# Kernel tuning notes

Measured on AMD Instinct MI355X. Metric: run time of the kernel, lower is better.

The kernel has to match this reference:

```python
import jax, jax.numpy as jnp
import numpy as np

N, IN_DIM, OUT_DIM, NUM_HOPS, SD = 8192, 256, 256, 4, 64
ETA, LAM_LAP, LAM_SP, EPS = 0.5, 0.3, 0.05, 0.5
LN_EPS = 1e-5


def setup_inputs() -> dict:
    key = jax.random.key(0)
    ks = jax.random.split(key, 6)
    K = NUM_HOPS + 1
    return {
        "H": jax.random.normal(ks[0], (N, IN_DIM), jnp.float32),
        "hops": jax.random.normal(ks[1], (K, N, IN_DIM), jnp.float32),
        "L": jax.random.normal(ks[2], (N, N), jnp.float32),
        "U": jax.random.normal(ks[3], (K, IN_DIM, SD), jnp.float32) * 0.1,
        "W_in": jax.random.normal(ks[4], (OUT_DIM, IN_DIM), jnp.float32) * 0.05,
        "ln_gamma": jnp.ones((OUT_DIM,), jnp.float32),
        "ln_beta": jnp.zeros((OUT_DIM,), jnp.float32),
        "log_tau": jnp.zeros((), jnp.float32),
    }


def _per_hop(U_k, H_k):
    n = H_k.shape[0]
    Q, _ = jnp.linalg.qr(U_k)                 # [in_dim, sd]
    Z = Q.T @ H_k.T                           # [sd, n]
    G = Z @ Z.T                               # [sd, sd] Gram, reused
    Sigma = G / (n + 1e-8)
    tr_S = jnp.trace(Sigma)
    tr_S2 = jnp.sum(Sigma * Sigma)            # trace(Sigma @ Sigma), Sigma symmetric
    rank_eff = tr_S ** 2 / (tr_S2 + 1e-8)
    coeff = SD / (n * EPS ** 2 + 1e-8)
    M = jnp.eye(SD, dtype=Z.dtype) + coeff * G
    Lc = jnp.linalg.cholesky(M)
    MiZ = jax.scipy.linalg.cho_solve((Lc, True), Z)  # [sd, n]
    grad_R = (Q @ MiZ).T                      # [n, in_dim]
    return rank_eff, grad_R


def reference(H, hops, L, U, W_in, ln_gamma, ln_beta, log_tau):
    tau = jnp.clip(jnp.exp(log_tau), 0.1, 10.0)
    rank_effs, grads_R = jax.vmap(_per_hop)(U, hops)      # [K], [K,n,in_dim]
    lap_terms = jnp.einsum('nm,kmd->knd', L, hops)        # [K,n,in_dim]
    w = jax.nn.softmax(rank_effs / tau)                   # [K]
    grad_sum = jnp.einsum('k,knd->nd', w, grads_R)
    lap_sum = jnp.einsum('k,knd->nd', w, lap_terms)
    H_half = H + ETA * grad_sum - ETA * LAM_LAP * lap_sum
    H_prox = jnp.sign(H_half) * jax.nn.relu(jnp.abs(H_half) - LAM_SP * ETA)
    H_out = H_prox @ W_in.T
    mu = jnp.mean(H_out, axis=-1, keepdims=True)
    var = jnp.var(H_out, axis=-1, keepdims=True)
    H_out = (H_out - mu) * jax.lax.rsqrt(var + LN_EPS) * ln_gamma + ln_beta
    return H_out, rank_effs, w
```

## Files before the change

### kernel.cpp

```cpp
#include <hip/hip_runtime.h>
#include <stdint.h>


typedef __attribute__((ext_vector_type(8))) short  s16x8;
typedef __attribute__((ext_vector_type(4))) float  f32x4;

#define NNODE 8192
#define DIN   256
#define KHOP  5
#define SDM   64

static const size_t OFF_Q    = 0;
static const size_t OFF_QT   = OFF_Q   + (size_t)5*256*64*4;
static const size_t OFF_ZT   = OFF_QT  + (size_t)5*64*256*2;
static const size_t OFF_GP   = OFF_ZT  + (size_t)5*8192*64*2;
static const size_t OFF_LM   = OFF_GP  + (size_t)5*16*4096*4;
static const size_t OFF_RD   = OFF_LM  + (size_t)5*4096*4;
static const size_t OFF_LU   = OFF_RD  + (size_t)5*64*4;
static const size_t OFF_RDU  = OFF_LU  + (size_t)5*4096*4;
static const size_t OFF_RE   = OFF_RDU + (size_t)5*64*4;
static const size_t OFF_W    = OFF_RE  + 64;
static const size_t OFF_T2   = OFF_W   + 64;
static const size_t OFF_HWT  = OFF_T2  + (size_t)5*256*64*2;
static const size_t OFF_WBF  = OFF_HWT + (size_t)256*8192*2;
static const size_t OFF_HP   = OFF_WBF + (size_t)256*256*2;
static const size_t OFF_PART = OFF_HP  + (size_t)8192*256*2;

__device__ __forceinline__ unsigned short f2bf(float f){
  unsigned u = __builtin_bit_cast(unsigned, f);
  u += 0x7FFFu + ((u >> 16) & 1u);
  return (unsigned short)(u >> 16);
}
__device__ __forceinline__ float bf2f(unsigned h){
  return __builtin_bit_cast(float, h << 16);
}
__device__ __forceinline__ void gl_lds16(const void* g, void* l){
  __builtin_amdgcn_global_load_lds(
      (const __attribute__((address_space(1))) void*)g,
      (__attribute__((address_space(3))) void*)l, 16, 0, 0);
}
__device__ __forceinline__ f32x4 mfma16(s16x8 a, s16x8 b, f32x4 c){
  return __builtin_amdgcn_mfma_f32_16x16x32_bf16(a, b, c, 0, 0, 0);
}

__device__ __forceinline__ void wave_chol64(float* a, float& rdk, int lane){
  rdk = 0.0f;
  #pragma unroll
  for (int j = 0; j < 64; ++j){
    float dj  = __shfl(a[j], j);
    float d   = sqrtf(fmaxf(dj, 1e-20f));
    float rdj = 1.0f / d;
    float cj  = a[j] * rdj;
    a[j] = cj;
    if (lane == j) rdk = rdj;
    #pragma unroll
    for (int l = j+1; l < 64; ++l)
      a[l] -= cj * __shfl(cj, l);
  }
}

__global__ __launch_bounds__(256) void k_pre(const float* __restrict__ U,
                                             float* __restrict__ Lu,
                                             float* __restrict__ rdu){
  __shared__ float A[64*65];
  int tid = threadIdx.x;
  int k = blockIdx.x;
  const float* Uk = U + (size_t)k*16384;
  int ti = tid >> 4, tj = tid & 15;
  float s[16];
  #pragma unroll
  for (int i = 0; i < 16; ++i) s[i] = 0.0f;
  for (int n = 0; n < 256; ++n){
    f32x4 xa = *(const f32x4*)(Uk + n*64 + ti*4);
    f32x4 xb = *(const f32x4*)(Uk + n*64 + tj*4);
    #pragma unroll
    for (int p = 0; p < 4; ++p)
      #pragma unroll
      for (int q = 0; q < 4; ++q) s[p*4+q] += xa[p]*xb[q];
  }
  #pragma unroll
  for (int p = 0; p < 4; ++p)
    #pragma unroll
    for (int q = 0; q < 4; ++q) A[(ti*4+p)*65 + tj*4+q] = s[p*4+q];
  __syncthreads();
  if (tid < 64){
    int lane = tid;
    float a[64];
    #pragma unroll
    for (int l = 0; l < 64; ++l) a[l] = A[lane*65 + l];
    float rdk;
    wave_chol64(a, rdk, lane);
    #pragma unroll
    for (int l = 0; l < 64; ++l) Lu[(size_t)k*4096 + lane*64 + l] = a[l];
    rdu[k*64 + lane] = rdk;
  }
}

__global__ __launch_bounds__(256) void k_qsolve(const float* __restrict__ U,
                                                const float* __restrict__ Lu,
                                                const float* __restrict__ rdu,
                                                float* __restrict__ Qf,
                                                unsigned short* __restrict__ Qt){
  int k = blockIdx.y, tid = threadIdx.x, wave = tid >> 6, lane = tid & 63;
  __shared__ float Al[64*65];
  __shared__ float rds[64];
  for (int e = tid; e < 4096; e += 256) Al[(e>>6)*65 + (e&63)] = Lu[(size_t)k*4096 + e];
  if (tid < 64) rds[tid] = rdu[k*64 + tid];
  __syncthreads();
  int n = blockIdx.x*4 + wave;
  float x = U[((size_t)k*256 + n)*64 + lane];
  #pragma unroll
  for (int j = 0; j < 64; ++j){
    float zj = __shfl(x, j) * rds[j];
    x = (lane == j) ? zj : (lane > j ? x - Al[lane*65+j]*zj : x);
  }
  Qf[((size_t)k*256 + n)*64 + lane] = x;
  Qt[(size_t)k*16384 + lane*256 + n] = f2bf(x);
}

__global__ __launch_bounds__(256,2) void k_zgemm(const float* __restrict__ hops,
                                                 const unsigned short* __restrict__ Qt,
                                                 unsigned short* __restrict__ Zt){
  __shared__ __align__(16) unsigned short Al[128][72];
  __shared__ __align__(16) unsigned short Bl[64][64];
  int tid = threadIdx.x, lane = tid & 63, wave = tid >> 6;
  int q = lane >> 4, r = lane & 15;
  int k = blockIdx.y, m0 = blockIdx.x * 128;
  f32x4 acc[2][4];
  #pragma unroll
  for (int a = 0; a < 2; ++a)
    #pragma unroll
    for (int b = 0; b < 4; ++b) acc[a][b] = (f32x4){0,0,0,0};
  int rr = tid >> 1, half = tid & 1;
  for (int it = 0; it < 4; ++it){
    __syncthreads();
    #pragma unroll
    for (int i = 0; i < 2; ++i){
      int o = i*4096 + wave*1024 + lane*16;
      int srow = o >> 7, kc = (o & 127) >> 1;
      gl_lds16(Qt + (size_t)k*16384 + srow*256 + it*64 + kc,
               (char*)&Bl[0][0] + i*4096 + wave*1024);
    }
    const float* ga = hops + ((size_t)k*NNODE + m0 + rr)*256 + it*64 + half*32;
    f32x4 v[8];
    #pragma unroll
    for (int i = 0; i < 8; ++i) v[i] = *(const f32x4*)(ga + i*4);
    #pragma unroll
    for (int i = 0; i < 4; ++i){
      s16x8 t;
      #pragma unroll
      for (int j = 0; j < 8; ++j){ int e = i*8+j; t[j] = (short)f2bf(v[e>>2][e&3]); }
      *(s16x8*)&Al[rr][half*32 + i*8] = t;
    }
    __syncthreads();
    #pragma unroll
    for (int h = 0; h < 2; ++h){
      int ko = h*32 + q*8;
      s16x8 b[4];
      #pragma unroll
      for (int ni = 0; ni < 4; ++ni) b[ni] = *(const s16x8*)&Bl[ni*16 + r][ko];
      #pragma unroll
      for (int mi = 0; mi < 2; ++mi){
        s16x8 a = *(const s16x8*)&Al[wave*32 + mi*16 + r][ko];
        #pragma unroll
        for (int ni = 0; ni < 4; ++ni) acc[mi][ni] = mfma16(a, b[ni], acc[mi][ni]);
      }
    }
  }
  #pragma unroll
  for (int mi = 0; mi < 2; ++mi)
    #pragma unroll
    for (int ni = 0; ni < 4; ++ni)
      #pragma unroll
      for (int ii = 0; ii < 4; ++ii){
        int m = m0 + wave*32 + mi*16 + q*4 + ii;
        int sc = ni*16 + r;
        Zt[((size_t)k*NNODE + m)*64 + sc] = f2bf(acc[mi][ni][ii]);
      }
}

__global__ __launch_bounds__(256) void k_gpart(const unsigned short* __restrict__ Zt,
                                               float* __restrict__ Gp){
  int k = blockIdx.x, c = blockIdx.y, tid = threadIdx.x;
  __shared__ __align__(16) unsigned short Zl[128][64];
  int ti = tid >> 4, tj = tid & 15;
  float acc[16];
  #pragma unroll
  for (int i = 0; i < 16; ++i) acc[i] = 0.0f;
  for (int sub = 0; sub < 4; ++sub){
    const char* gb = (const char*)Zt + ((size_t)k*NNODE + c*512 + sub*128)*128;
    __syncthreads();
    #pragma unroll
    for (int i = 0; i < 4; ++i){
      int o = i*4096 + tid*16;
      *(uint4*)((char*)&Zl[0][0] + o) = *(const uint4*)(gb + o);
    }
    __syncthreads();
    for (int n = 0; n < 128; ++n){
      const unsigned short* row = &Zl[n][0];
      uint2 ua = *(const uint2*)(row + ti*4);
      uint2 ub = *(const uint2*)(row + tj*4);
      float xa[4] = { bf2f(ua.x & 0xffff), bf2f(ua.x >> 16), bf2f(ua.y & 0xffff), bf2f(ua.y >> 16) };
      float xb[4] = { bf2f(ub.x & 0xffff), bf2f(ub.x >> 16), bf2f(ub.y & 0xffff), bf2f(ub.y >> 16) };
      #pragma unroll
      for (int p = 0; p < 4; ++p)
        #pragma unroll
        for (int qn = 0; qn < 4; ++qn) acc[p*4+qn] += xa[p]*xb[qn];
    }
  }
  float* o = Gp + ((size_t)k*16 + c)*4096;
  #pragma unroll
  for (int p = 0; p < 4; ++p)
    #pragma unroll
    for (int qn = 0; qn < 4; ++qn) o[(ti*4+p)*64 + tj*4+qn] = acc[p*4+qn];
}

__global__ __launch_bounds__(256) void k_gred(const float* __restrict__ Gp,
                                              float* __restrict__ LmO,
                                              float* __restrict__ rdO,
                                              float* __restrict__ reO){
  int k = blockIdx.x, tid = threadIdx.x;
  __shared__ float A[64*65];
  __shared__ float red[256];
  int ti = tid >> 4, tj = tid & 15;
  float s[16];
  #pragma unroll
  for (int i = 0; i < 16; ++i) s[i] = 0.0f;
  for (int c = 0; c < 16; ++c){
    const float* g = Gp + ((size_t)k*16 + c)*4096 + (ti*4)*64 + tj*4;
    #pragma unroll
    for (int p = 0; p < 4; ++p)
      #pragma unroll
      for (int qn = 0; qn < 4; ++qn) s[p*4+qn] += g[p*64+qn];
  }
  const float sc    = 1.0f / (8192.0f + 1e-8f);
  const float coeff = 64.0f / (8192.0f*0.25f + 1e-8f);
  float trp = 0.0f, tr2p = 0.0f;
  #pragma unroll
  for (int p = 0; p < 4; ++p)
    #pragma unroll
    for (int qn = 0; qn < 4; ++qn){
      float gg = s[p*4+qn];
      float sg = gg * sc;
      tr2p += sg*sg;
      int row = ti*4+p, col = tj*4+qn;
      if (row == col) trp += sg;
      A[row*65 + col] = (row == col ? 1.0f : 0.0f) + coeff*gg;
    }
  red[tid] = trp; __syncthreads();
  for (int o = 128; o > 0; o >>= 1){ if (tid < o) red[tid] += red[tid+o]; __syncthreads(); }
  float tr = red[0]; __syncthreads();
  red[tid] = tr2p; __syncthreads();
  for (int o = 128; o > 0; o >>= 1){ if (tid < o) red[tid] += red[tid+o]; __syncthreads(); }
  float tr2 = red[0];
  if (tid == 0) reO[k] = tr*tr / (tr2 + 1e-8f);
  __syncthreads();
  if (tid < 64){
    int lane = tid;
    float a[64];
    #pragma unroll
    for (int l = 0; l < 64; ++l) a[l] = A[lane*65 + l];
    float rdk;
    wave_chol64(a, rdk, lane);
    #pragma unroll
    for (int l = 0; l < 64; ++l) LmO[(size_t)k*4096 + lane*64 + l] = a[l];
    rdO[k*64 + lane] = rdk;
  }
}

__global__ void k_soft(const float* __restrict__ re, const float* __restrict__ ltau,
                       float* __restrict__ wv, float* __restrict__ dtail){
  if (threadIdx.x == 0){
    float tau = expf(ltau[0]);
    tau = fminf(fmaxf(tau, 0.1f), 10.0f);
    float r[5], m = -1e30f;
    for (int i = 0; i < 5; ++i){ r[i] = re[i]; m = fmaxf(m, r[i]); }
    float e[5], sum = 0.0f;
    for (int i = 0; i < 5; ++i){ e[i] = expf((r[i]-m)/tau); sum += e[i]; }
    for (int i = 0; i < 5; ++i){
      float w = e[i]/sum;
      wv[i] = w; dtail[i] = r[i]; dtail[5+i] = w;
    }
  }
}

__global__ __launch_bounds__(256) void k_post(const float* __restrict__ hops,
                                              const float* __restrict__ wv,
                                              unsigned short* __restrict__ hwT,
                                              const float* __restrict__ Qf,
                                              const float* __restrict__ LmI,
                                              const float* __restrict__ rdI,
                                              unsigned short* __restrict__ T2w,
                                              const float* __restrict__ Win,
                                              unsigned short* __restrict__ Wbf){
  __shared__ float T[64*65];
  __shared__ float rds[64];
  int bid = blockIdx.x, tid = threadIdx.x;
  if (bid < 512){
    int n0 = (bid & 127)*64, d0 = (bid >> 7)*64;
    float wl[5];
    #pragma unroll
    for (int k = 0; k < 5; ++k) wl[k] = -0.15f * wv[k];
    for (int e = tid; e < 1024; e += 256){
      int row = e >> 4, c4 = (e & 15)*4;
      f32x4 acc = (f32x4){0,0,0,0};
      #pragma unroll
      for (int k = 0; k < 5; ++k){
        f32x4 v = *(const f32x4*)(hops + ((size_t)k*NNODE + n0 + row)*256 + d0 + c4);
        acc += v * wl[k];
      }
      T[row*65 + c4+0] = acc[0]; T[row*65 + c4+1] = acc[1];
      T[row*65 + c4+2] = acc[2]; T[row*65 + c4+3] = acc[3];
    }
    __syncthreads();
    for (int e = tid; e < 1024; e += 256){
      int dr = e >> 4, c4 = (e & 15)*4;
      unsigned short h0 = f2bf(T[(c4+0)*65 + dr]);
      unsigned short h1 = f2bf(T[(c4+1)*65 + dr]);
      unsigned short h2 = f2bf(T[(c4+2)*65 + dr]);
      unsigned short h3 = f2bf(T[(c4+3)*65 + dr]);
      uint2 u; u.x = (unsigned)h0 | ((unsigned)h1 << 16); u.y = (unsigned)h2 | ((unsigned)h3 << 16);
      *(uint2*)(hwT + (size_t)(d0+dr)*NNODE + n0 + c4) = u;
    }
  } else if (bid < 832){
    int i = bid - 512;
    int k = i >> 6, xb = i & 63;
    int wave = tid >> 6, lane = tid & 63;
    for (int e = tid; e < 4096; e += 256) T[(e>>6)*65 + (e&63)] = LmI[(size_t)k*4096 + e];
    if (tid < 64) rds[tid] = rdI[k*64 + tid];
    __syncthreads();
    int n = xb*4 + wave;
    float x = Qf[((size_t)k*256 + n)*64 + lane];
    #pragma unroll
    for (int j = 0; j < 64; ++j){
      float zj = __shfl(x, j) * rds[j];
      x = (lane == j) ? zj : (lane > j ? x - T[lane*65+j]*zj : x);
    }
    #pragma unroll
    for (int j = 63; j >= 0; --j){
      float yj = __shfl(x, j) * rds[j];
      x = (lane == j) ? yj : (lane < j ? x - T[j*65+lane]*yj : x);
    }
    float scale = 0.5f * wv[k];
    T2w[((size_t)k*256 + n)*64 + lane] = f2bf(scale * x);
  } else {
    int i = bid - 832;
    int e = (i*256 + tid)*4;
    f32x4 v = *(const f32x4*)(Win + e);
    uint2 u;
    u.x = (unsigned)f2bf(v[0]) | ((unsigned)f2bf(v[1]) << 16);
    u.y = (unsigned)f2bf(v[2]) | ((unsigned)f2bf(v[3]) << 16);
    *(uint2*)(Wbf + e) = u;
  }
}

__global__ __launch_bounds__(256,1) void k_gg(const float* __restrict__ Lf,
                                              const unsigned short* __restrict__ Bt,
                                              unsigned short* __restrict__ part,
                                              const unsigned short* __restrict__ Zt,
                                              const unsigned short* __restrict__ T2w){
  __shared__ __align__(16) unsigned short SM[49920];
  int bid = blockIdx.x, tid = threadIdx.x;
  int lane = tid & 63, wave = tid >> 6;
  int q = lane >> 4, r = lane & 15;
  if (bid < 512){
    unsigned short* A0 = SM;
    unsigned short* B0 = SM + 16*520;
    unsigned short* A1 = SM + 48*520;
    unsigned short* B1 = SM + 64*520;
    int m0 = (bid & 63) * 128;
    int by = bid >> 6;
    size_t kbase = (size_t)by * 1024;
    int sr = lane >> 3, sc8 = (lane & 7) * 8;
    f32x4 acc[8][4];
    #pragma unroll
    for (int a = 0; a < 8; ++a)
      #pragma unroll
      for (int b = 0; b < 4; ++b) acc[a][b] = (f32x4){0,0,0,0};
    {
      f32x4 av[4][2];
      #pragma unroll
      for (int i = 0; i < 4; ++i){
        int c = i*4 + wave;
        const float* p = Lf + (size_t)(m0 + c*8 + sr)*NNODE + kbase + sc8;
        av[i][0] = *(const f32x4*)p;
        av[i][1] = *(const f32x4*)(p + 4);
      }
      #pragma unroll
      for (int i = 0; i < 8; ++i){
        int cb = i*4 + wave;
        gl_lds16(Bt + (size_t)(cb*8 + sr)*NNODE + kbase + sc8,
                 (char*)B0 + cb*1040 + lane*16);
      }
      #pragma unroll
      for (int i = 0; i < 4; ++i){
        int c = i*4 + wave;
        s16x8 t;
        #pragma unroll
        for (int e = 0; e < 8; ++e) t[e] = (short)f2bf(av[i][e>>2][e&3]);
        *(s16x8*)((char*)A0 + c*1040 + lane*16) = t;
      }
      __syncthreads();
    }
    for (int t = 0; t < 16; ++t){
      unsigned short* Ac = (t & 1) ? A1 : A0;
      unsigned short* Bc = (t & 1) ? B1 : B0;
      unsigned short* An = (t & 1) ? A0 : A1;
      unsigned short* Bn = (t & 1) ? B0 : B1;
      size_t kn = kbase + (size_t)(t+1)*64;
      f32x4 av[4][2];
      if (t < 15){
        #pragma unroll
        for (int i = 0; i < 4; ++i){
          int c = i*4 + wave;
          const float* p = Lf + (size_t)(m0 + c*8 + sr)*NNODE + kn + sc8;
          av[i][0] = *(const f32x4*)p;
          av[i][1] = *(const f32x4*)(p + 4);
        }
        #pragma unroll
        for (int i = 0; i < 8; ++i){
          int cb = i*4 + wave;
          gl_lds16(Bt + (size_t)(cb*8 + sr)*NNODE + kn + sc8,
                   (char*)Bn + cb*1040 + lane*16);
        }
      }
      #pragma unroll
      for (int h = 0; h < 2; ++h){
        int ko = h*32 + q*8;
        s16x8 b[4];
        #pragma unroll
        for (int ni = 0; ni < 4; ++ni){
          int d = wave*64 + ni*16 + r;
          b[ni] = *(const s16x8*)(Bc + (d>>3)*520 + (d&7)*64 + ko);
        }
        #pragma unroll
        for (int mi = 0; mi < 8; ++mi){
          int m = mi*16 + r;
          s16x8 a = *(const s16x8*)(Ac + (m>>3)*520 + (m&7)*64 + ko);
          #pragma unroll
          for (int ni = 0; ni < 4; ++ni) acc[mi][ni] = mfma16(a, b[ni], acc[mi][ni]);
        }
      }
      if (t < 15){
        #pragma unroll
        for (int i = 0; i < 4; ++i){
          int c = i*4 + wave;
          s16x8 tt;
          #pragma unroll
          for (int e = 0; e < 8; ++e) tt[e] = (short)f2bf(av[i][e>>2][e&3]);
          *(s16x8*)((char*)An + c*1040 + lane*16) = tt;
        }
      }
      __syncthreads();
    }
    unsigned short* o = part + (size_t)by * 2097152;
    #pragma unroll
    for (int mi = 0; mi < 8; ++mi)
      #pragma unroll
      for (int ni = 0; ni < 4; ++ni)
        #pragma unroll
        for (int ii = 0; ii < 4; ++ii){
          int m = m0 + mi*16 + q*4 + ii;
          int n = wave*64 + ni*16 + r;
          o[(size_t)m*256 + n] = f2bf(acc[mi][ni][ii]);
        }
  } else {
    unsigned short* Al = SM;
    unsigned short* Bl = SM + 2048;
    int m0 = (bid - 512) * 32;
    f32x4 acc[2][4];
    #pragma unroll
    for (int a = 0; a < 2; ++a)
      #pragma unroll
      for (int b = 0; b < 4; ++b) acc[a][b] = (f32x4){0,0,0,0};
    for (int kk = 0; kk < 5; ++kk){
      __syncthreads();
      {
        int o = wave*1024 + lane*16;
        gl_lds16((const char*)Zt + ((size_t)kk*NNODE + m0)*128 + o,
                 (char*)Al + wave*1024);
      }
      #pragma unroll
      for (int i = 0; i < 8; ++i){
        int o = i*4096 + wave*1024 + lane*16;
        gl_lds16((const char*)T2w + (size_t)kk*32768 + o,
                 (char*)Bl + i*4096 + wave*1024);
      }
      __syncthreads();
      #pragma unroll
      for (int h = 0; h < 2; ++h){
        int ko = h*32 + q*8;
        s16x8 b[4];
        #pragma unroll
        for (int ni = 0; ni < 4; ++ni) b[ni] = *(const s16x8*)&Bl[(wave*64 + ni*16 + r)*64 + ko];
        #pragma unroll
        for (int mi = 0; mi < 2; ++mi){
          s16x8 a = *(const s16x8*)&Al[(mi*16 + r)*64 + ko];
          #pragma unroll
          for (int ni = 0; ni < 4; ++ni) acc[mi][ni] = mfma16(a, b[ni], acc[mi][ni]);
        }
      }
    }
    unsigned short* o8 = part + (size_t)8 * 2097152;
    #pragma unroll
    for (int mi = 0; mi < 2; ++mi)
      #pragma unroll
      for (int ni = 0; ni < 4; ++ni)
        #pragma unroll
        for (int ii = 0; ii < 4; ++ii){
          int m = m0 + mi*16 + q*4 + ii;
          int n = wave*64 + ni*16 + r;
          o8[(size_t)m*256 + n] = f2bf(acc[mi][ni][ii]);
        }
  }
}

__global__ __launch_bounds__(256,2) void k_finln(const float* __restrict__ H,
                                                 const unsigned short* __restrict__ part,
                                                 const unsigned short* __restrict__ Wbf,
                                                 const float* __restrict__ gamma,
                                                 const float* __restrict__ beta,
                                                 float* __restrict__ out){
  __shared__ __align__(16) unsigned short Hl[64][264];
  __shared__ __align__(16) unsigned short Bl[256][64];
  __shared__ float SmR[64][4];
  __shared__ float SqR[64][4];
  int tid = threadIdx.x, lane = tid & 63, wave = tid >> 6;
  int q = lane >> 4, r = lane & 15;
  int m0 = blockIdx.x * 64;
  #define PROX(a) ({ float _t = fabsf(a) - 0.025f; _t > 0.0f ? copysignf(_t,(a)) : 0.0f; })
  for (int g = tid; g < 4096; g += 256){
    int row = g >> 6, c4 = (g & 63) * 4;
    size_t e = (size_t)(m0 + row)*256 + c4;
    f32x4 h = *(const f32x4*)(H + e);
    float s0 = h[0], s1 = h[1], s2 = h[2], s3 = h[3];
    #pragma unroll
    for (int sl = 0; sl < 9; ++sl){
      uint2 u = *(const uint2*)(part + (size_t)sl*2097152 + e);
      s0 += bf2f(u.x & 0xffff); s1 += bf2f(u.x >> 16);
      s2 += bf2f(u.y & 0xffff); s3 += bf2f(u.y >> 16);
    }
    uint2 o;
    o.x = (unsigned)f2bf(PROX(s0)) | ((unsigned)f2bf(PROX(s1)) << 16);
    o.y = (unsigned)f2bf(PROX(s2)) | ((unsigned)f2bf(PROX(s3)) << 16);
    *(uint2*)&Hl[row][c4] = o;
  }
  f32x4 acc[4][4];
  #pragma unroll
  for (int a = 0; a < 4; ++a)
    #pragma unroll
    for (int b = 0; b < 4; ++b) acc[a][b] = (f32x4){0,0,0,0};
  for (int it = 0; it < 4; ++it){
    __syncthreads();
    #pragma unroll
    for (int i = 0; i < 8; ++i){
      int o = i*4096 + wave*1024 + lane*16;
      int n = o >> 7, kc = o & 127;
      gl_lds16((const char*)Wbf + (size_t)n*512 + it*128 + kc,
               (char*)&Bl[0][0] + i*4096 + wave*1024);
    }
    __syncthreads();
    #pragma unroll
    for (int h = 0; h < 2; ++h){
      int ko = it*64 + h*32 + q*8;
      s16x8 b[4];
      #pragma unroll
      for (int ni = 0; ni < 4; ++ni) b[ni] = *(const s16x8*)&Bl[wave*64 + ni*16 + r][h*32 + q*8];
      #pragma unroll
      for (int mi = 0; mi < 4; ++mi){
        s16x8 a = *(const s16x8*)&Hl[mi*16 + r][ko];
        #pragma unroll
        for (int ni = 0; ni < 4; ++ni) acc[mi][ni] = mfma16(a, b[ni], acc[mi][ni]);
      }
    }
  }
  #pragma unroll
  for (int mi = 0; mi < 4; ++mi)
    #pragma unroll
    for (int ii = 0; ii < 4; ++ii){
      float sm = 0.0f, sq = 0.0f;
      #pragma unroll
      for (int ni = 0; ni < 4; ++ni){
        float v = acc[mi][ni][ii];
        sm += v; sq += v*v;
      }
      #pragma unroll
      for (int o = 1; o < 16; o <<= 1){ sm += __shfl_xor(sm, o, 64); sq += __shfl_xor(sq, o, 64); }
      if (r == 0){
        int rl = mi*16 + q*4 + ii;
        SmR[rl][wave] = sm; SqR[rl][wave] = sq;
      }
    }
  __syncthreads();
  float g[4], b[4];
  #pragma unroll
  for (int ni = 0; ni < 4; ++ni){
    g[ni] = gamma[wave*64 + ni*16 + r];
    b[ni] = beta [wave*64 + ni*16 + r];
  }
  #pragma unroll
  for (int mi = 0; mi < 4; ++mi)
    #pragma unroll
    for (int ii = 0; ii < 4; ++ii){
      int rl = mi*16 + q*4 + ii;
      float sm = SmR[rl][0] + SmR[rl][1] + SmR[rl][2] + SmR[rl][3];
      float sq = SqR[rl][0] + SqR[rl][1] + SqR[rl][2] + SqR[rl][3];
      float mean = sm * (1.0f/256.0f);
      float var  = sq * (1.0f/256.0f) - mean*mean;
      float rs   = rsqrtf(var + 1e-5f);
      #pragma unroll
      for (int ni = 0; ni < 4; ++ni){
        out[(size_t)(m0+rl)*256 + wave*64 + ni*16 + r] =
            (acc[mi][ni][ii] - mean)*rs*g[ni] + b[ni];
      }
    }
}

extern "C" void kernel_launch(void* const* d_in, const int* in_sizes, int n_in,
                              void* d_out, int out_size, void* d_ws, size_t ws_size,
                              hipStream_t stream){
  const float* H    = (const float*)d_in[0];
  const float* hops = (const float*)d_in[1];
  const float* Lmat = (const float*)d_in[2];
  const float* U    = (const float*)d_in[3];
  const float* Win  = (const float*)d_in[4];
  const float* gam  = (const float*)d_in[5];
  const float* bet  = (const float*)d_in[6];
  const float* ltau = (const float*)d_in[7];
  float* out = (float*)d_out;

  char* ws = (char*)d_ws;
  float*          Qf   = (float*)(ws + OFF_Q);
  unsigned short* Qt   = (unsigned short*)(ws + OFF_QT);
  unsigned short* Zt   = (unsigned short*)(ws + OFF_ZT);
  float*          Gp   = (float*)(ws + OFF_GP);
  float*          Lm   = (float*)(ws + OFF_LM);
  float*          rdw  = (float*)(ws + OFF_RD);
  float*          Lu   = (float*)(ws + OFF_LU);
  float*          rdu  = (float*)(ws + OFF_RDU);
  float*          re   = (float*)(ws + OFF_RE);
  float*          wv   = (float*)(ws + OFF_W);
  unsigned short* T2w  = (unsigned short*)(ws + OFF_T2);
  unsigned short* hwT  = (unsigned short*)(ws + OFF_HWT);
  unsigned short* Wbf  = (unsigned short*)(ws + OFF_WBF);
  unsigned short* part = (unsigned short*)(ws + OFF_PART);

  hipLaunchKernelGGL(k_pre,    dim3(5),      dim3(256), 0, stream, U, Lu, rdu);
  hipLaunchKernelGGL(k_qsolve, dim3(64,5),   dim3(256), 0, stream, U, Lu, rdu, Qf, Qt);
  hipLaunchKernelGGL(k_zgemm,  dim3(64,5),   dim3(256), 0, stream, hops, Qt, Zt);
  hipLaunchKernelGGL(k_gpart,  dim3(5,16),   dim3(256), 0, stream, Zt, Gp);
  hipLaunchKernelGGL(k_gred,   dim3(5),      dim3(256), 0, stream, Gp, Lm, rdw, re);
  hipLaunchKernelGGL(k_soft,   dim3(1),      dim3(64),  0, stream, re, ltau, wv, out + 2097152);
  hipLaunchKernelGGL(k_post,   dim3(896),    dim3(256), 0, stream, hops, wv, hwT, Qf, Lm, rdw, T2w, Win, Wbf);
  hipLaunchKernelGGL(k_gg,     dim3(768),    dim3(256), 0, stream, Lmat, hwT, part, Zt, T2w);
  hipLaunchKernelGGL(k_finln,  dim3(128),    dim3(256), 0, stream, H, part, Wbf, gam, bet, out);
}
```

Before: 662.2 us.

## Single-buffer LDS with XOR swizzle in L-GEMM to raise occupancy

The L·hops GEMM blocks drop double-buffered LDS for a single half-size buffer and add an XOR swizzle on both A and B tiles to avoid LDS bank conflicts. Launch bounds rise from 1 to 3 blocks per CU. The intent is to hide latency with more resident blocks instead of in-block double buffering. In exchange the loop now has an extra barrier per K step and loses overlap of global-to-LDS copies with MFMA inside a block. Register pressure under the tighter bound (32 accumulator vectors) may cause spills.

```diff
diff --git a/kernel.cpp b/kernel.cpp
--- a/kernel.cpp
+++ b/kernel.cpp
@@ -42,6 +42,9 @@
 __device__ __forceinline__ f32x4 mfma16(s16x8 a, s16x8 b, f32x4 c){
   return __builtin_amdgcn_mfma_f32_16x16x32_bf16(a, b, c, 0, 0, 0);
 }
+__device__ __forceinline__ int swz(int row7, int colbyte){
+  return row7*128 + (colbyte ^ (row7 << 4));
+}
 
 __device__ __forceinline__ void wave_chol64(float* a, float& rdk, int lane){
   rdk = 0.0f;
@@ -354,24 +357,25 @@
   }
 }
 
-__global__ __launch_bounds__(256,1) void k_gg(const float* __restrict__ Lf,
+__global__ __launch_bounds__(256,3) void k_gg(const float* __restrict__ Lf,
                                               const unsigned short* __restrict__ Bt,
                                               unsigned short* __restrict__ part,
                                               const unsigned short* __restrict__ Zt,
                                               const unsigned short* __restrict__ T2w){
-  __shared__ __align__(16) unsigned short SM[49920];
+  __shared__ __align__(16) unsigned short SM[24960];
   int bid = blockIdx.x, tid = threadIdx.x;
   int lane = tid & 63, wave = tid >> 6;
   int q = lane >> 4, r = lane & 15;
   if (bid < 512){
-    unsigned short* A0 = SM;
-    unsigned short* B0 = SM + 16*520;
-    unsigned short* A1 = SM + 48*520;
-    unsigned short* B1 = SM + 64*520;
+    char* Al = (char*)SM;
+    char* Bl = (char*)SM + 16*1040;
     int m0 = (bid & 63) * 128;
     int by = bid >> 6;
     size_t kbase = (size_t)by * 1024;
-    int sr = lane >> 3, sc8 = (lane & 7) * 8;
+    int sr = lane >> 3;
+    int sc8b = ((lane & 7) ^ sr) * 8;
+    int sc8a = (lane & 7) * 8;
+    int adst = swz(sr, (lane & 7) * 16);
     f32x4 acc[8][4];
     #pragma unroll
     for (int a = 0; a < 8; ++a)
@@ -382,15 +386,15 @@
       #pragma unroll
       for (int i = 0; i < 4; ++i){
         int c = i*4 + wave;
-        const float* p = Lf + (size_t)(m0 + c*8 + sr)*NNODE + kbase + sc8;
+        const float* p = Lf + (size_t)(m0 + c*8 + sr)*NNODE + kbase + sc8a;
         av[i][0] = *(const f32x4*)p;
         av[i][1] = *(const f32x4*)(p + 4);
       }
       #pragma unroll
       for (int i = 0; i < 8; ++i){
         int cb = i*4 + wave;
-        gl_lds16(Bt + (size_t)(cb*8 + sr)*NNODE + kbase + sc8,
-                 (char*)B0 + cb*1040 + lane*16);
+        gl_lds16(Bt + (size_t)(cb*8 + sr)*NNODE + kbase + sc8b,
+                 Bl + cb*1040 + lane*16);
       }
       #pragma unroll
       for (int i = 0; i < 4; ++i){
@@ -398,57 +402,54 @@
         s16x8 t;
         #pragma unroll
         for (int e = 0; e < 8; ++e) t[e] = (short)f2bf(av[i][e>>2][e&3]);
-        *(s16x8*)((char*)A0 + c*1040 + lane*16) = t;
+        *(s16x8*)(Al + c*1040 + adst) = t;
       }
       __syncthreads();
     }
     for (int t = 0; t < 16; ++t){
-      unsigned short* Ac = (t & 1) ? A1 : A0;
-      unsigned short* Bc = (t & 1) ? B1 : B0;
-      unsigned short* An = (t & 1) ? A0 : A1;
-      unsigned short* Bn = (t & 1) ? B0 : B1;
       size_t kn = kbase + (size_t)(t+1)*64;
       f32x4 av[4][2];
       if (t < 15){
         #pragma unroll
         for (int i = 0; i < 4; ++i){
           int c = i*4 + wave;
-          const float* p = Lf + (size_t)(m0 + c*8 + sr)*NNODE + kn + sc8;
+          const float* p = Lf + (size_t)(m0 + c*8 + sr)*NNODE + kn + sc8a;
           av[i][0] = *(const f32x4*)p;
           av[i][1] = *(const f32x4*)(p + 4);
         }
+      }
+      #pragma unroll
+      for (int h = 0; h < 2; ++h){
+        int kb = h*64 + q*16;
+        s16x8 b[4];
+        #pragma unroll
+        for (int ni = 0; ni < 4; ++ni){
+          int d = wave*64 + ni*16 + r;
+          b[ni] = *(const s16x8*)(Bl + (d>>3)*1040 + swz(d&7, kb));
+        }
+        #pragma unroll
+        for (int mi = 0; mi < 8; ++mi){
+          int m = mi*16 + r;
+          s16x8 a = *(const s16x8*)(Al + (m>>3)*1040 + swz(m&7, kb));
+          #pragma unroll
+          for (int ni = 0; ni < 4; ++ni) acc[mi][ni] = mfma16(a, b[ni], acc[mi][ni]);
+        }
+      }
+      __syncthreads();
+      if (t < 15){
         #pragma unroll
         for (int i = 0; i < 8; ++i){
           int cb = i*4 + wave;
-          gl_lds16(Bt + (size_t)(cb*8 + sr)*NNODE + kn + sc8,
-                   (char*)Bn + cb*1040 + lane*16);
-        }
-      }
-      #pragma unroll
-      for (int h = 0; h < 2; ++h){
-        int ko = h*32 + q*8;
-        s16x8 b[4];
-        #pragma unroll
-        for (int ni = 0; ni < 4; ++ni){
-          int d = wave*64 + ni*16 + r;
-          b[ni] = *(const s16x8*)(Bc + (d>>3)*520 + (d&7)*64 + ko);
-        }
-        #pragma unroll
-        for (int mi = 0; mi < 8; ++mi){
-          int m = mi*16 + r;
-          s16x8 a = *(const s16x8*)(Ac + (m>>3)*520 + (m&7)*64 + ko);
-          #pragma unroll
-          for (int ni = 0; ni < 4; ++ni) acc[mi][ni] = mfma16(a, b[ni], acc[mi][ni]);
-        }
-      }
-      if (t < 15){
+          gl_lds16(Bt + (size_t)(cb*8 + sr)*NNODE + kn + sc8b,
+                   Bl + cb*1040 + lane*16);
+        }
         #pragma unroll
         for (int i = 0; i < 4; ++i){
           int c = i*4 + wave;
           s16x8 tt;
           #pragma unroll
           for (int e = 0; e < 8; ++e) tt[e] = (short)f2bf(av[i][e>>2][e&3]);
-          *(s16x8*)((char*)An + c*1040 + lane*16) = tt;
+          *(s16x8*)(Al + c*1040 + adst) = tt;
         }
       }
       __syncthreads();
```

Result: slower. 735.4 us (+11.1%).
